# Kernel optimization log

Hardware: AMD Instinct MI355X
Metric: run time of the kernel (lower is better)

The kernel has to match this reference:

```python
import jax, jax.numpy as jnp
import numpy as np

EMB = 64      # per-head dim (emb_dim in source)
HEADS = 8
D = EMB * HEADS          # 512, model width
FF = 4 * EMB             # 256 (source uses ff_hidden_mult*emb_dim, not *D)
BS, NE = 32, 512
EPS = 1e-5


def _layernorm(x, g, b):
    mu = jnp.mean(x, axis=-1, keepdims=True)
    var = jnp.mean((x - mu) ** 2, axis=-1, keepdims=True)
    return (x - mu) * jax.lax.rsqrt(var + EPS) * g + b


def setup_inputs() -> dict:
    key = jax.random.key(0)
    ks = jax.random.split(key, 8)
    w = lambda k, shape: jax.random.normal(k, shape, jnp.float32) * 0.02
    return {
        "x": jax.random.normal(ks[0], (BS, NE, D), jnp.float32),
        "Wq": w(ks[1], (D, D)), "bq": jnp.zeros((D,), jnp.float32),
        "Wk": w(ks[2], (D, D)), "bk": jnp.zeros((D,), jnp.float32),
        "Wv": w(ks[3], (D, D)), "bv": jnp.zeros((D,), jnp.float32),
        "W1": w(ks[4], (D, FF)), "bf1": jnp.zeros((FF,), jnp.float32),
        "W2": w(ks[5], (FF, D)), "bf2": jnp.zeros((D,), jnp.float32),
        "g1": jnp.ones((D,), jnp.float32), "be1": jnp.zeros((D,), jnp.float32),
        "g2": jnp.ones((D,), jnp.float32), "be2": jnp.zeros((D,), jnp.float32),
    }


def reference(x, Wq, bq, Wk, bk, Wv, bv, W1, bf1, W2, bf2, g1, be1, g2, be2):
    bs, ne, _ = x.shape
    # --- SelfAttention.forward_i (manual multi-head attention) ---
    q = (x @ Wq + bq).reshape(bs, ne, HEADS, EMB)
    k = (x @ Wk + bk).reshape(bs, ne, HEADS, EMB)
    v = (x @ Wv + bv).reshape(bs, ne, HEADS, EMB)
    scores = jnp.einsum("bqhd,bkhd->bhqk", q, k) / jnp.sqrt(jnp.float32(EMB))
    att = jax.nn.softmax(scores, axis=-1)
    attended = jnp.einsum("bhqk,bkhd->bqhd", att, v).reshape(bs * ne, D)
    # --- TransformerBlock residual + LN + FF + LN ---
    xf = x.reshape(bs * ne, D)
    h = _layernorm(attended + xf, g1, be1)
    ff = jnp.maximum(h @ W1 + bf1, 0.0) @ W2 + bf2
    return _layernorm(ff + h, g2, be2)
```

## Files before the change

kernel.cpp:

```cpp
#include <hip/hip_runtime.h>

#define BS 32
#define NE 512
#define DMODEL 512
#define HEADS 8
#define EMB 64
#define FFH 256
#define MTOK (BS*NE)

typedef unsigned short u16;
typedef short v8s __attribute__((ext_vector_type(8)));
typedef float f32x4 __attribute__((ext_vector_type(4)));
typedef u16 u16x4 __attribute__((ext_vector_type(4)));

#define GLOAD16(G, L) \
  __builtin_amdgcn_global_load_lds((const __attribute__((address_space(1))) unsigned int*)(G), \
      (__attribute__((address_space(3))) unsigned int*)(L), 16, 0, 0)

static __device__ __forceinline__ unsigned cvt_pk_bf16(float lo, float hi) {
    unsigned r;
    asm("v_cvt_pk_bf16_f32 %0, %1, %2" : "=v"(r) : "v"(lo), "v"(hi));
    return r;
}

static __device__ __forceinline__ u16 f2bf_bits(float f) {
    unsigned u = __float_as_uint(f);
    u += 0x7fffu + ((u >> 16) & 1u);
    return (u16)(u >> 16);
}
static __device__ __forceinline__ float bflo(unsigned w) { return __uint_as_float(w << 16); }
static __device__ __forceinline__ float bfhi(unsigned w) { return __uint_as_float(w & 0xffff0000u); }

__global__ __launch_bounds__(256) void cvt_all_kernel(
    const float* __restrict__ x, u16* __restrict__ xb,
    const float* __restrict__ Wq, const float* __restrict__ Wk, const float* __restrict__ Wv,
    const float* __restrict__ W1, const float* __restrict__ W2,
    u16* __restrict__ WqkvT, u16* __restrict__ W1T, u16* __restrict__ W2T)
{
    const int id = blockIdx.x;
    const int tt = threadIdx.x;
    if (id < 8192) {
        int i = id*256 + tt;
        float4 v = ((const float4*)x)[i];
        u16x4 o = { f2bf_bits(v.x), f2bf_bits(v.y), f2bf_bits(v.z), f2bf_bits(v.w) };
        ((u16x4*)xb)[i] = o;
        return;
    }
    __shared__ float T[32][33];
    const int tid2 = id - 8192;
    const float* src; u16* dst; int ldsrc, lddst, sr, sc;
    if (tid2 < 768) {
        int w = tid2 >> 8, t = tid2 & 255;
        int tr = t >> 4, tc = t & 15;
        src = (w == 0) ? Wq : (w == 1) ? Wk : Wv;
        ldsrc = 512; sr = tr*32; sc = tc*32;
        dst = WqkvT + (size_t)(w*512 + sc)*512 + sr; lddst = 512;
    } else if (tid2 < 896) {
        int t = tid2 - 768;
        int tr = t >> 3, tc = t & 7;
        src = W1; ldsrc = 256; sr = tr*32; sc = tc*32;
        dst = W1T + (size_t)sc*512 + sr; lddst = 512;
    } else {
        int t = tid2 - 896;
        int tr = t >> 4, tc = t & 15;
        src = W2; ldsrc = 512; sr = tr*32; sc = tc*32;
        dst = W2T + (size_t)sc*256 + sr; lddst = 256;
    }
    {
        int r = tt >> 3, c4 = (tt & 7) << 2;
        float4 v = *(const float4*)(src + (size_t)(sr + r)*ldsrc + sc + c4);
        T[r][c4] = v.x; T[r][c4+1] = v.y; T[r][c4+2] = v.z; T[r][c4+3] = v.w;
    }
    __syncthreads();
    {
        int n = tt >> 3, k4 = (tt & 7) << 2;
        u16x4 o = { f2bf_bits(T[k4][n]), f2bf_bits(T[k4+1][n]),
                    f2bf_bits(T[k4+2][n]), f2bf_bits(T[k4+3][n]) };
        *(u16x4*)(dst + (size_t)n*lddst + k4) = o;
    }
}

__global__ __launch_bounds__(256, 2) void qkv_kernel(
    const u16* __restrict__ A, const u16* __restrict__ BT,
    const float* __restrict__ bsQ, const float* __restrict__ bsK, const float* __restrict__ bsV,
    u16* __restrict__ oQ, u16* __restrict__ oK, u16* __restrict__ oVT)
{
    __shared__ u16 Ab[2][128*64];
    __shared__ u16 Bb[2][128*64];
    const int tid = threadIdx.x;
    const int wave = tid >> 6, lane = tid & 63;
    const int lr = lane & 15, lg = lane >> 4, lr7 = lr & 7;
    const int id = blockIdx.x;
    const int rr = id & 7, qq = id >> 3;
    const int gk = qq / 12, colBlk = qq - gk*12;
    const int rowBlk = gk*8 + rr;
    const int aRow0 = rowBlk*128, bRow0 = colBlk*128;
    const int wlo = (wave >> 1)*64, wco = (wave & 1)*64;
    const int srow = tid >> 3, schunk = tid & 7;
    const int soff = ((schunk ^ (srow & 7)) << 3);
    const bool isV = (bRow0 >= 1024);

    auto stage = [&](int bsel, int k0) {
        #pragma unroll
        for (int i = 0; i < 4; ++i) {
            int row = i*32 + srow;
            GLOAD16(A  + (size_t)(aRow0 + row)*512 + k0 + soff, (char*)&Ab[bsel][0] + i*4096 + wave*1024);
            GLOAD16(BT + (size_t)(bRow0 + row)*512 + k0 + soff, (char*)&Bb[bsel][0] + i*4096 + wave*1024);
        }
    };

    stage(0, 0);

    f32x4 acc[4][4] = {};
    #pragma unroll
    for (int t = 0; t < 8; ++t) {
        const int cur = t & 1;
        asm volatile("s_waitcnt vmcnt(0)" ::: "memory");
        __builtin_amdgcn_s_barrier();
        if (t + 1 < 8) stage(cur ^ 1, (t + 1) * 64);
        #pragma unroll
        for (int kk = 0; kk < 2; ++kk) {
            v8s af[4], bf[4];
            #pragma unroll
            for (int i = 0; i < 4; ++i) {
                af[i] = *(const v8s*)((const char*)&Ab[cur][0] + (wlo + i*16 + lr)*128 + ((((kk<<2)|lg) ^ lr7) << 4));
                bf[i] = *(const v8s*)((const char*)&Bb[cur][0] + (wco + i*16 + lr)*128 + ((((kk<<2)|lg) ^ lr7) << 4));
            }
            if (isV) {
                #pragma unroll
                for (int i = 0; i < 4; ++i)
                    #pragma unroll
                    for (int j = 0; j < 4; ++j)
                        acc[i][j] = __builtin_amdgcn_mfma_f32_16x16x32_bf16(af[i], bf[j], acc[i][j], 0, 0, 0);
            } else {
                #pragma unroll
                for (int i = 0; i < 4; ++i)
                    #pragma unroll
                    for (int j = 0; j < 4; ++j)
                        acc[i][j] = __builtin_amdgcn_mfma_f32_16x16x32_bf16(bf[j], af[i], acc[i][j], 0, 0, 0);
            }
        }
    }

    if (isV) {
        #pragma unroll
        for (int j = 0; j < 4; ++j) {
            int col = (bRow0 & 511) + wco + j*16 + lr;
            float bv = bsV[col];
            int hh = col >> 6, d = col & 63;
            #pragma unroll
            for (int i = 0; i < 4; ++i) {
                int t0 = aRow0 + wlo + i*16 + lg*4;
                int bb = t0 >> 9, tr = t0 & 511;
                unsigned lo = cvt_pk_bf16(acc[i][j][0] + bv, acc[i][j][1] + bv);
                unsigned hi = cvt_pk_bf16(acc[i][j][2] + bv, acc[i][j][3] + bv);
                *(uint2*)(oVT + ((size_t)((bb*HEADS + hh)*EMB + d))*NE + tr) = make_uint2(lo, hi);
            }
        }
    } else {
        const int sel = (bRow0 >> 9) & 1;
        u16* dst = sel ? oK : oQ;
        const float* bias = sel ? bsK : bsQ;
        const int cb = bRow0 & 511;
        #pragma unroll
        for (int j = 0; j < 4; ++j) {
            int col0 = cb + wco + j*16 + lg*4;
            float4 b4 = *(const float4*)&bias[col0];
            #pragma unroll
            for (int i = 0; i < 4; ++i) {
                int row = aRow0 + wlo + i*16 + lr;
                float v0 = acc[i][j][0] + b4.x, v1 = acc[i][j][1] + b4.y;
                float v2 = acc[i][j][2] + b4.z, v3 = acc[i][j][3] + b4.w;
                if (sel == 0) {
                    const float SCL = 0.18033688011112042f;
                    v0 *= SCL; v1 *= SCL; v2 *= SCL; v3 *= SCL;
                }
                *(uint2*)(dst + (size_t)row*DMODEL + col0)
                    = make_uint2(cvt_pk_bf16(v0, v1), cvt_pk_bf16(v2, v3));
            }
        }
    }
}

__global__ __launch_bounds__(512, 2) void attn_kernel(
    const u16* __restrict__ Q, const u16* __restrict__ Kb,
    const u16* __restrict__ VT, u16* __restrict__ O)
{
    extern __shared__ char smem[];
    const int b = blockIdx.x >> 3, h = blockIdx.x & 7;
    const int tid = threadIdx.x, wave = tid >> 6, lane = tid & 63;
    const int lr = lane & 15, lg = lane >> 4, lr7 = lr & 7;

    const int srow = tid >> 3, schunk = tid & 7;
    const int soff = ((schunk ^ (srow & 7)) << 3);
    #pragma unroll
    for (int i = 0; i < 8; ++i)
        GLOAD16(Kb + (size_t)(b*NE + i*64 + srow)*DMODEL + h*EMB + soff,
                (char*)smem + i*8192 + wave*1024);
    #pragma unroll
    for (int i = 0; i < 8; ++i) {
        int row = i*8 + wave;
        GLOAD16(VT + (size_t)((b*HEADS + h)*EMB + row)*NE + lane*8,
                (char*)smem + 65536 + row*1040);
    }

    const int q0 = wave*64;
    v8s qa[4][2];
    #pragma unroll
    for (int ti = 0; ti < 4; ++ti) {
        const u16* qr = Q + (size_t)(b*NE + q0 + ti*16 + lr)*DMODEL + h*EMB;
        qa[ti][0] = *(const v8s*)(qr + lg*8);
        qa[ti][1] = *(const v8s*)(qr + 32 + lg*8);
    }
    __syncthreads();

    f32x4 o[4][4] = {};
    float ssum[4] = {0.f, 0.f, 0.f, 0.f};

    #pragma unroll 1
    for (int c = 0; c < 16; ++c) {
        const char* kr0 = (const char*)smem + ((2*c  )*16 + lr)*128;
        const char* kr1 = (const char*)smem + ((2*c+1)*16 + lr)*128;
        v8s kA0 = *(const v8s*)(kr0 + ((lg ^ lr7) << 4));
        v8s kA1 = *(const v8s*)(kr0 + (((4|lg) ^ lr7) << 4));
        v8s kB0 = *(const v8s*)(kr1 + ((lg ^ lr7) << 4));
        v8s kB1 = *(const v8s*)(kr1 + (((4|lg) ^ lr7) << 4));
        v8s vf[4];
        #pragma unroll
        for (int dt = 0; dt < 4; ++dt) {
            const char* vr = (const char*)smem + 65536 + (dt*16 + lr)*1040 + c*64 + lg*8;
            uint2 lo = *(const uint2*)(vr);
            uint2 hi = *(const uint2*)(vr + 32);
            uint4 u = make_uint4(lo.x, lo.y, hi.x, hi.y);
            vf[dt] = *(v8s*)&u;
        }
        #pragma unroll
        for (int ti = 0; ti < 4; ++ti) {
            __builtin_amdgcn_s_setprio(1);
            f32x4 s0 = {0.f,0.f,0.f,0.f}, s1 = {0.f,0.f,0.f,0.f};
            s0 = __builtin_amdgcn_mfma_f32_16x16x32_bf16(kA0, qa[ti][0], s0, 0, 0, 0);
            s0 = __builtin_amdgcn_mfma_f32_16x16x32_bf16(kA1, qa[ti][1], s0, 0, 0, 0);
            s1 = __builtin_amdgcn_mfma_f32_16x16x32_bf16(kB0, qa[ti][0], s1, 0, 0, 0);
            s1 = __builtin_amdgcn_mfma_f32_16x16x32_bf16(kB1, qa[ti][1], s1, 0, 0, 0);
            __builtin_amdgcn_s_setprio(0);
            float p0 = exp2f(s0[0]), p1 = exp2f(s0[1]), p2 = exp2f(s0[2]), p3 = exp2f(s0[3]);
            float r0 = exp2f(s1[0]), r1 = exp2f(s1[1]), r2 = exp2f(s1[2]), r3 = exp2f(s1[3]);
            ssum[ti] += ((p0 + p1) + (p2 + p3)) + ((r0 + r1) + (r2 + r3));
            unsigned a0 = cvt_pk_bf16(p0, p1), a1 = cvt_pk_bf16(p2, p3);
            unsigned b0 = cvt_pk_bf16(r0, r1), b1 = cvt_pk_bf16(r2, r3);
            uint4 pu = make_uint4(a0, a1, b0, b1);
            v8s pb = *(v8s*)&pu;
            __builtin_amdgcn_s_setprio(1);
            #pragma unroll
            for (int dt = 0; dt < 4; ++dt)
                o[ti][dt] = __builtin_amdgcn_mfma_f32_16x16x32_bf16(vf[dt], pb, o[ti][dt], 0, 0, 0);
            __builtin_amdgcn_s_setprio(0);
        }
    }

    __syncthreads();

    float rinv[4];
    #pragma unroll
    for (int ti = 0; ti < 4; ++ti) {
        float v = ssum[ti];
        v += __shfl_xor(v, 16);
        v += __shfl_xor(v, 32);
        rinv[ti] = 1.f / v;
    }

    char* ow = (char*)smem + wave*10240;
    #pragma unroll
    for (int ti = 0; ti < 4; ++ti) {
        #pragma unroll
        for (int dt = 0; dt < 4; ++dt) {
            unsigned d0 = cvt_pk_bf16(o[ti][dt][0]*rinv[ti], o[ti][dt][1]*rinv[ti]);
            unsigned d1 = cvt_pk_bf16(o[ti][dt][2]*rinv[ti], o[ti][dt][3]*rinv[ti]);
            *(uint2*)(ow + (ti*16 + lr)*160 + dt*32 + lg*8) = make_uint2(d0, d1);
        }
    }
    __asm__ volatile("s_waitcnt lgkmcnt(0)" ::: "memory");
    #pragma unroll
    for (int it = 0; it < 8; ++it) {
        int rr2 = it*8 + (lane >> 3);
        uint4 v = *(const uint4*)(ow + rr2*160 + (lane & 7)*16);
        *(uint4*)(O + (size_t)(b*NE + q0 + rr2)*DMODEL + h*EMB + (lane & 7)*8) = v;
    }
}

__global__ __launch_bounds__(512) void ffln_kernel(
    const u16* __restrict__ At, const u16* __restrict__ xb,
    const float* __restrict__ g1, const float* __restrict__ be1,
    const u16* __restrict__ W1T, const float* __restrict__ b1,
    const u16* __restrict__ W2T, const float* __restrict__ b2,
    const float* __restrict__ g2, const float* __restrict__ be2,
    float* __restrict__ out)
{
    extern __shared__ char smem[];
    char* H    = smem;
    char* F1   = smem + 65536;
    char* BSTa = smem + 98304;
    float* Ps = (float*)(smem + 131072);
    float* Pq = Ps + 128;

    const int tid = threadIdx.x, wave = tid >> 6, lane = tid & 63;
    const int lr = lane & 15, lg = lane >> 4, lr7 = lr & 7;
    const int r0 = blockIdx.x * 64;

    #pragma unroll
    for (int it = 0; it < 8; ++it) {
        int r = wave*8 + it;
        uint4 av = *(const uint4*)(At + (size_t)(r0 + r)*512 + lane*8);
        uint4 xv = *(const uint4*)(xb + (size_t)(r0 + r)*512 + lane*8);
        float v0 = bflo(av.x) + bflo(xv.x), v1 = bfhi(av.x) + bfhi(xv.x);
        float v2 = bflo(av.y) + bflo(xv.y), v3 = bfhi(av.y) + bfhi(xv.y);
        float v4 = bflo(av.z) + bflo(xv.z), v5 = bfhi(av.z) + bfhi(xv.z);
        float v6 = bflo(av.w) + bflo(xv.w), v7 = bfhi(av.w) + bfhi(xv.w);
        float s = ((v0+v1)+(v2+v3)) + ((v4+v5)+(v6+v7));
        float q = ((v0*v0+v1*v1)+(v2*v2+v3*v3)) + ((v4*v4+v5*v5)+(v6*v6+v7*v7));
        #pragma unroll
        for (int d = 1; d < 64; d <<= 1) { s += __shfl_xor(s, d); q += __shfl_xor(q, d); }
        float mu = s * (1.f/512.f);
        float rs = rsqrtf(q * (1.f/512.f) - mu*mu + 1e-5f);
        float4 gA = *(const float4*)(g1 + lane*8), gB = *(const float4*)(g1 + lane*8 + 4);
        float4 eA = *(const float4*)(be1 + lane*8), eB = *(const float4*)(be1 + lane*8 + 4);
        float h0 = (v0-mu)*rs*gA.x + eA.x, h1 = (v1-mu)*rs*gA.y + eA.y;
        float h2 = (v2-mu)*rs*gA.z + eA.z, h3 = (v3-mu)*rs*gA.w + eA.w;
        float h4 = (v4-mu)*rs*gB.x + eB.x, h5 = (v5-mu)*rs*gB.y + eB.y;
        float h6 = (v6-mu)*rs*gB.z + eB.z, h7 = (v7-mu)*rs*gB.w + eB.w;
        uint4 hw = make_uint4(cvt_pk_bf16(h0,h1), cvt_pk_bf16(h2,h3),
                              cvt_pk_bf16(h4,h5), cvt_pk_bf16(h6,h7));
        *(uint4*)(H + r*1024 + ((lane ^ (r & 7)) << 4)) = hw;
    }
    __syncthreads();

    const int wr = (wave & 3)*16, wcB = (wave >> 2)*128;

    auto stageW1 = [&](char* buf, int s8) {
        int k0 = s8*64;
        #pragma unroll
        for (int i = 0; i < 4; ++i) {
            int slot = i*512 + tid;
            int row = slot >> 3, ch = slot & 7;
            GLOAD16(W1T + (size_t)row*512 + k0 + ((ch ^ (row & 7)) << 3),
                    buf + i*8192 + wave*1024);
        }
    };
    stageW1(BSTa, 0);
    f32x4 acc1[8] = {};
    #pragma unroll
    for (int s8 = 0; s8 < 8; ++s8) {
        char* cur = (s8 & 1) ? F1 : BSTa;
        asm volatile("s_waitcnt vmcnt(0)" ::: "memory");
        __builtin_amdgcn_s_barrier();
        if (s8 + 1 < 8) stageW1((s8 & 1) ? BSTa : F1, s8 + 1);
        #pragma unroll
        for (int kk = 0; kk < 2; ++kk) {
            v8s af = *(const v8s*)(H + (wr + lr)*1024 + (((s8*8 + kk*4 + lg) ^ lr7) << 4));
            v8s bf[8];
            #pragma unroll
            for (int j = 0; j < 8; ++j)
                bf[j] = *(const v8s*)(cur + (wcB + j*16 + lr)*128 + ((((kk<<2)|lg) ^ lr7) << 4));
            #pragma unroll
            for (int j = 0; j < 8; ++j)
                acc1[j] = __builtin_amdgcn_mfma_f32_16x16x32_bf16(bf[j], af, acc1[j], 0, 0, 0);
        }
    }
    __syncthreads();

    {
        int row = wr + lr;
        #pragma unroll
        for (int j = 0; j < 8; ++j) {
            int col0 = wcB + j*16 + lg*4;
            float4 b4 = *(const float4*)(b1 + col0);
            float v0 = fmaxf(acc1[j][0] + b4.x, 0.f), v1 = fmaxf(acc1[j][1] + b4.y, 0.f);
            float v2 = fmaxf(acc1[j][2] + b4.z, 0.f), v3 = fmaxf(acc1[j][3] + b4.w, 0.f);
            *(uint2*)(F1 + row*512 + (((col0 >> 3) ^ (row & 7)) << 4) + (col0 & 7)*2)
                = make_uint2(cvt_pk_bf16(v0, v1), cvt_pk_bf16(v2, v3));
        }
    }

    const int row = wr + lr;
    uint2 hres[2][8];
    #pragma unroll
    for (int nh = 0; nh < 2; ++nh)
        #pragma unroll
        for (int j = 0; j < 8; ++j) {
            int col0 = nh*256 + wcB + j*16 + lg*4;
            hres[nh][j] = *(const uint2*)(H + row*1024 +
                            ((((col0 & 511) >> 3) ^ (row & 7)) << 4) + (col0 & 7)*2);
        }
    __syncthreads();

    auto stageW2 = [&](char* buf, int g) {
        int nh = g >> 2, k0 = (g & 3)*64;
        #pragma unroll
        for (int i = 0; i < 4; ++i) {
            int slot = i*512 + tid;
            int rw = slot >> 3, ch = slot & 7;
            GLOAD16(W2T + (size_t)(nh*256 + rw)*256 + k0 + ((ch ^ (rw & 7)) << 3),
                    buf + i*8192 + wave*1024);
        }
    };
    stageW2(H, 0);
    f32x4 acc2[2][8] = {};
    #pragma unroll
    for (int g = 0; g < 8; ++g) {
        char* cur = (g & 1) ? (H + 32768) : H;
        asm volatile("s_waitcnt vmcnt(0)" ::: "memory");
        __builtin_amdgcn_s_barrier();
        if (g + 1 < 8) stageW2((g & 1) ? H : (H + 32768), g + 1);
        const int nh = g >> 2, s4 = g & 3;
        #pragma unroll
        for (int kk = 0; kk < 2; ++kk) {
            v8s af = *(const v8s*)(F1 + (wr + lr)*512 + (((s4*8 + kk*4 + lg) ^ lr7) << 4));
            v8s bf[8];
            #pragma unroll
            for (int j = 0; j < 8; ++j)
                bf[j] = *(const v8s*)(cur + (wcB + j*16 + lr)*128 + ((((kk<<2)|lg) ^ lr7) << 4));
            #pragma unroll
            for (int j = 0; j < 8; ++j)
                acc2[nh][j] = __builtin_amdgcn_mfma_f32_16x16x32_bf16(bf[j], af, acc2[nh][j], 0, 0, 0);
        }
    }

    float s = 0.f, q = 0.f;
    #pragma unroll
    for (int nh = 0; nh < 2; ++nh) {
        #pragma unroll
        for (int j = 0; j < 8; ++j) {
            int col0 = nh*256 + wcB + j*16 + lg*4;
            float4 b4 = *(const float4*)(b2 + col0);
            uint2 hh = hres[nh][j];
            f32x4 a = acc2[nh][j];
            a[0] += b4.x + bflo(hh.x); a[1] += b4.y + bfhi(hh.x);
            a[2] += b4.z + bflo(hh.y); a[3] += b4.w + bfhi(hh.y);
            acc2[nh][j] = a;
            s += (a[0]+a[1]) + (a[2]+a[3]);
            q += (a[0]*a[0]+a[1]*a[1]) + (a[2]*a[2]+a[3]*a[3]);
        }
    }
    s += __shfl_xor(s, 16); s += __shfl_xor(s, 32);
    q += __shfl_xor(q, 16); q += __shfl_xor(q, 32);
    __syncthreads();
    if (lg == 0) { Ps[row*2 + (wave >> 2)] = s; Pq[row*2 + (wave >> 2)] = q; }
    __syncthreads();
    float st = Ps[row*2] + Ps[row*2 + 1];
    float qt = Pq[row*2] + Pq[row*2 + 1];
    float mu = st * (1.f/512.f);
    float rs = rsqrtf(qt * (1.f/512.f) - mu*mu + 1e-5f);

    #pragma unroll
    for (int nh = 0; nh < 2; ++nh) {
        #pragma unroll
        for (int j = 0; j < 8; ++j) {
            int col0 = nh*256 + wcB + j*16 + lg*4;
            float4 gg = *(const float4*)(g2 + col0);
            float4 ee = *(const float4*)(be2 + col0);
            f32x4 a = acc2[nh][j];
            float4 o;
            o.x = (a[0]-mu)*rs*gg.x + ee.x;
            o.y = (a[1]-mu)*rs*gg.y + ee.y;
            o.z = (a[2]-mu)*rs*gg.z + ee.z;
            o.w = (a[3]-mu)*rs*gg.w + ee.w;
            *(float4*)(out + (size_t)(r0 + row)*512 + col0) = o;
        }
    }
}


extern "C" void kernel_launch(void* const* d_in, const int* in_sizes, int n_in,
                              void* d_out, int out_size, void* d_ws, size_t ws_size,
                              hipStream_t stream)
{
    const float* x   = (const float*)d_in[0];
    const float* Wq  = (const float*)d_in[1];
    const float* bq  = (const float*)d_in[2];
    const float* Wk  = (const float*)d_in[3];
    const float* bk  = (const float*)d_in[4];
    const float* Wv  = (const float*)d_in[5];
    const float* bv  = (const float*)d_in[6];
    const float* W1  = (const float*)d_in[7];
    const float* bf1 = (const float*)d_in[8];
    const float* W2  = (const float*)d_in[9];
    const float* bf2 = (const float*)d_in[10];
    const float* g1  = (const float*)d_in[11];
    const float* be1 = (const float*)d_in[12];
    const float* g2  = (const float*)d_in[13];
    const float* be2 = (const float*)d_in[14];

    char* ws = (char*)d_ws;
    const size_t MB = 1ull << 20;
    const size_t KB = 1024;
    u16* xb    = (u16*)(ws + 0);
    u16* qb    = (u16*)(ws + 16*MB);
    u16* kb    = (u16*)(ws + 32*MB);
    u16* vT    = (u16*)(ws + 48*MB);
    u16* attnb = (u16*)(ws + 64*MB);
    u16* WqkvT = (u16*)(ws + 80*MB);
    u16* W1T   = (u16*)(ws + 80*MB + 1536*KB);
    u16* W2T   = (u16*)(ws + 80*MB + 1792*KB);
    (void)ws_size; (void)in_sizes; (void)n_in; (void)out_size;

    cvt_all_kernel<<<9216, 256, 0, stream>>>(x, xb, Wq, Wk, Wv, W1, W2, WqkvT, W1T, W2T);

    qkv_kernel<<<1536, 256, 0, stream>>>(xb, WqkvT, bq, bk, bv, qb, kb, vT);

    attn_kernel<<<256, 512, 132096, stream>>>(qb, kb, vT, attnb);

    ffln_kernel<<<256, 512, 132096, stream>>>(attnb, xb, g1, be1, W1T, bf1, W2T, bf2,
                                              g2, be2, (float*)d_out);
}
```

Measured before the change: 114.4 us.

## Fuse QKV projection into attention kernel using MFMA-fragment-packed inputs

Removes the separate QKV GEMM kernel and computes each head's Q, K and V projections inside the attention block. Q, K and V now go straight to LDS instead of round-tripping through global memory. To feed MFMA directly from global memory without LDS staging, x and Wqkv are repacked in the conversion kernel into a 16-row by 8-element fragment layout. Each block recomputes projections from global x with register double buffering. The trade-off is lower occupancy (launch bounds no longer request 2 blocks per CU), extra conversion writes, and global-load latency exposed inside the GEMM passes.

```diff
diff --git a/kernel.cpp b/kernel.cpp
--- a/kernel.cpp
+++ b/kernel.cpp
@@ -32,10 +32,10 @@
 static __device__ __forceinline__ float bfhi(unsigned w) { return __uint_as_float(w & 0xffff0000u); }
 
 __global__ __launch_bounds__(256) void cvt_all_kernel(
-    const float* __restrict__ x, u16* __restrict__ xb,
+    const float* __restrict__ x, u16* __restrict__ xb, u16* __restrict__ xp,
     const float* __restrict__ Wq, const float* __restrict__ Wk, const float* __restrict__ Wv,
     const float* __restrict__ W1, const float* __restrict__ W2,
-    u16* __restrict__ WqkvT, u16* __restrict__ W1T, u16* __restrict__ W2T)
+    u16* __restrict__ Wp, u16* __restrict__ W1T, u16* __restrict__ W2T)
 {
     const int id = blockIdx.x;
     const int tt = threadIdx.x;
@@ -44,24 +44,29 @@
         float4 v = ((const float4*)x)[i];
         u16x4 o = { f2bf_bits(v.x), f2bf_bits(v.y), f2bf_bits(v.z), f2bf_bits(v.w) };
         ((u16x4*)xb)[i] = o;
+        int e = i * 4;
+        int row = e >> 9, k = e & 511;
+        *(u16x4*)(xp + ((size_t)(row >> 4)*64 + (k >> 3))*128 + (row & 15)*8 + (k & 7)) = o;
         return;
     }
+    if (id < 11264) {
+        int widx = (id - 8192)*256 + tt;
+        int w = widx >> 18, rem = widx & 262143;
+        int k = rem >> 9, n = rem & 511;
+        const float* src = (w == 0) ? Wq : (w == 1) ? Wk : Wv;
+        int np = w*512 + n;
+        Wp[((size_t)(np >> 4)*64 + (k >> 3))*128 + (np & 15)*8 + (k & 7)] = f2bf_bits(src[rem]);
+        return;
+    }
     __shared__ float T[32][33];
-    const int tid2 = id - 8192;
+    const int t2 = id - 11264;
     const float* src; u16* dst; int ldsrc, lddst, sr, sc;
-    if (tid2 < 768) {
-        int w = tid2 >> 8, t = tid2 & 255;
-        int tr = t >> 4, tc = t & 15;
-        src = (w == 0) ? Wq : (w == 1) ? Wk : Wv;
-        ldsrc = 512; sr = tr*32; sc = tc*32;
-        dst = WqkvT + (size_t)(w*512 + sc)*512 + sr; lddst = 512;
-    } else if (tid2 < 896) {
-        int t = tid2 - 768;
-        int tr = t >> 3, tc = t & 7;
+    if (t2 < 128) {
+        int tr = t2 >> 3, tc = t2 & 7;
         src = W1; ldsrc = 256; sr = tr*32; sc = tc*32;
         dst = W1T + (size_t)sc*512 + sr; lddst = 512;
     } else {
-        int t = tid2 - 896;
+        int t = t2 - 128;
         int tr = t >> 4, tc = t & 15;
         src = W2; ldsrc = 512; sr = tr*32; sc = tc*32;
         dst = W2T + (size_t)sc*256 + sr; lddst = 256;
@@ -80,140 +85,118 @@
     }
 }
 
-__global__ __launch_bounds__(256, 2) void qkv_kernel(
-    const u16* __restrict__ A, const u16* __restrict__ BT,
+__global__ __launch_bounds__(512) void fused_attn_kernel(
+    const u16* __restrict__ xp, const u16* __restrict__ Wp,
     const float* __restrict__ bsQ, const float* __restrict__ bsK, const float* __restrict__ bsV,
-    u16* __restrict__ oQ, u16* __restrict__ oK, u16* __restrict__ oVT)
-{
-    __shared__ u16 Ab[2][128*64];
-    __shared__ u16 Bb[2][128*64];
-    const int tid = threadIdx.x;
-    const int wave = tid >> 6, lane = tid & 63;
-    const int lr = lane & 15, lg = lane >> 4, lr7 = lr & 7;
-    const int id = blockIdx.x;
-    const int rr = id & 7, qq = id >> 3;
-    const int gk = qq / 12, colBlk = qq - gk*12;
-    const int rowBlk = gk*8 + rr;
-    const int aRow0 = rowBlk*128, bRow0 = colBlk*128;
-    const int wlo = (wave >> 1)*64, wco = (wave & 1)*64;
-    const int srow = tid >> 3, schunk = tid & 7;
-    const int soff = ((schunk ^ (srow & 7)) << 3);
-    const bool isV = (bRow0 >= 1024);
-
-    auto stage = [&](int bsel, int k0) {
-        #pragma unroll
-        for (int i = 0; i < 4; ++i) {
-            int row = i*32 + srow;
-            GLOAD16(A  + (size_t)(aRow0 + row)*512 + k0 + soff, (char*)&Ab[bsel][0] + i*4096 + wave*1024);
-            GLOAD16(BT + (size_t)(bRow0 + row)*512 + k0 + soff, (char*)&Bb[bsel][0] + i*4096 + wave*1024);
-        }
-    };
-
-    stage(0, 0);
-
-    f32x4 acc[4][4] = {};
-    #pragma unroll
-    for (int t = 0; t < 8; ++t) {
-        const int cur = t & 1;
-        asm volatile("s_waitcnt vmcnt(0)" ::: "memory");
-        __builtin_amdgcn_s_barrier();
-        if (t + 1 < 8) stage(cur ^ 1, (t + 1) * 64);
-        #pragma unroll
-        for (int kk = 0; kk < 2; ++kk) {
-            v8s af[4], bf[4];
-            #pragma unroll
-            for (int i = 0; i < 4; ++i) {
-                af[i] = *(const v8s*)((const char*)&Ab[cur][0] + (wlo + i*16 + lr)*128 + ((((kk<<2)|lg) ^ lr7) << 4));
-                bf[i] = *(const v8s*)((const char*)&Bb[cur][0] + (wco + i*16 + lr)*128 + ((((kk<<2)|lg) ^ lr7) << 4));
-            }
-            if (isV) {
-                #pragma unroll
-                for (int i = 0; i < 4; ++i)
-                    #pragma unroll
-                    for (int j = 0; j < 4; ++j)
-                        acc[i][j] = __builtin_amdgcn_mfma_f32_16x16x32_bf16(af[i], bf[j], acc[i][j], 0, 0, 0);
-            } else {
-                #pragma unroll
-                for (int i = 0; i < 4; ++i)
-                    #pragma unroll
-                    for (int j = 0; j < 4; ++j)
-                        acc[i][j] = __builtin_amdgcn_mfma_f32_16x16x32_bf16(bf[j], af[i], acc[i][j], 0, 0, 0);
-            }
-        }
-    }
-
-    if (isV) {
-        #pragma unroll
-        for (int j = 0; j < 4; ++j) {
-            int col = (bRow0 & 511) + wco + j*16 + lr;
-            float bv = bsV[col];
-            int hh = col >> 6, d = col & 63;
-            #pragma unroll
-            for (int i = 0; i < 4; ++i) {
-                int t0 = aRow0 + wlo + i*16 + lg*4;
-                int bb = t0 >> 9, tr = t0 & 511;
-                unsigned lo = cvt_pk_bf16(acc[i][j][0] + bv, acc[i][j][1] + bv);
-                unsigned hi = cvt_pk_bf16(acc[i][j][2] + bv, acc[i][j][3] + bv);
-                *(uint2*)(oVT + ((size_t)((bb*HEADS + hh)*EMB + d))*NE + tr) = make_uint2(lo, hi);
-            }
-        }
-    } else {
-        const int sel = (bRow0 >> 9) & 1;
-        u16* dst = sel ? oK : oQ;
-        const float* bias = sel ? bsK : bsQ;
-        const int cb = bRow0 & 511;
-        #pragma unroll
-        for (int j = 0; j < 4; ++j) {
-            int col0 = cb + wco + j*16 + lg*4;
-            float4 b4 = *(const float4*)&bias[col0];
-            #pragma unroll
-            for (int i = 0; i < 4; ++i) {
-                int row = aRow0 + wlo + i*16 + lr;
-                float v0 = acc[i][j][0] + b4.x, v1 = acc[i][j][1] + b4.y;
-                float v2 = acc[i][j][2] + b4.z, v3 = acc[i][j][3] + b4.w;
-                if (sel == 0) {
-                    const float SCL = 0.18033688011112042f;
-                    v0 *= SCL; v1 *= SCL; v2 *= SCL; v3 *= SCL;
-                }
-                *(uint2*)(dst + (size_t)row*DMODEL + col0)
-                    = make_uint2(cvt_pk_bf16(v0, v1), cvt_pk_bf16(v2, v3));
-            }
-        }
-    }
-}
-
-__global__ __launch_bounds__(512, 2) void attn_kernel(
-    const u16* __restrict__ Q, const u16* __restrict__ Kb,
-    const u16* __restrict__ VT, u16* __restrict__ O)
+    u16* __restrict__ O)
 {
     extern __shared__ char smem[];
     const int b = blockIdx.x >> 3, h = blockIdx.x & 7;
     const int tid = threadIdx.x, wave = tid >> 6, lane = tid & 63;
     const int lr = lane & 15, lg = lane >> 4, lr7 = lr & 7;
-
-    const int srow = tid >> 3, schunk = tid & 7;
-    const int soff = ((schunk ^ (srow & 7)) << 3);
-    #pragma unroll
-    for (int i = 0; i < 8; ++i)
-        GLOAD16(Kb + (size_t)(b*NE + i*64 + srow)*DMODEL + h*EMB + soff,
-                (char*)smem + i*8192 + wave*1024);
-    #pragma unroll
-    for (int i = 0; i < 8; ++i) {
-        int row = i*8 + wave;
-        GLOAD16(VT + (size_t)((b*HEADS + h)*EMB + row)*NE + lane*8,
-                (char*)smem + 65536 + row*1040);
-    }
+    char* Bnc = smem + 65536;
+    const float SCL = 0.18033688011112042f;
+
+    const u16* a0  = xp + ((size_t)(b*32 + wave*4)*64 + lg)*128 + lr*8;
+    const u16* bq0 = Wp + ((size_t)(h*4      )*64 + lg)*128 + lr*8;
+    const u16* bk0 = Wp + ((size_t)(32 + h*4 )*64 + lg)*128 + lr*8;
+    const u16* bv0 = Wp + ((size_t)(64 + h*4 )*64 + lg)*128 + lr*8;
+
+    f32x4 acc[4][4];
+
+    auto run_pass = [&](const u16* bb, bool swap) {
+        #pragma unroll
+        for (int i = 0; i < 4; ++i)
+            #pragma unroll
+            for (int j = 0; j < 4; ++j) acc[i][j] = f32x4{0.f,0.f,0.f,0.f};
+        v8s afA[4], bfA[4], afB[4], bfB[4];
+        #pragma unroll
+        for (int i = 0; i < 4; ++i) { afA[i] = *(const v8s*)(a0 + i*8192); bfA[i] = *(const v8s*)(bb + i*8192); }
+        #pragma unroll
+        for (int tp = 0; tp < 8; ++tp) {
+            #pragma unroll
+            for (int i = 0; i < 4; ++i) {
+                afB[i] = *(const v8s*)(a0 + (2*tp + 1)*512 + i*8192);
+                bfB[i] = *(const v8s*)(bb + (2*tp + 1)*512 + i*8192);
+            }
+            #pragma unroll
+            for (int i = 0; i < 4; ++i)
+                #pragma unroll
+                for (int j = 0; j < 4; ++j)
+                    acc[i][j] = swap
+                        ? __builtin_amdgcn_mfma_f32_16x16x32_bf16(bfA[j], afA[i], acc[i][j], 0, 0, 0)
+                        : __builtin_amdgcn_mfma_f32_16x16x32_bf16(afA[i], bfA[j], acc[i][j], 0, 0, 0);
+            if (tp < 7) {
+                #pragma unroll
+                for (int i = 0; i < 4; ++i) {
+                    afA[i] = *(const v8s*)(a0 + (2*tp + 2)*512 + i*8192);
+                    bfA[i] = *(const v8s*)(bb + (2*tp + 2)*512 + i*8192);
+                }
+            }
+            #pragma unroll
+            for (int i = 0; i < 4; ++i)
+                #pragma unroll
+                for (int j = 0; j < 4; ++j)
+                    acc[i][j] = swap
+                        ? __builtin_amdgcn_mfma_f32_16x16x32_bf16(bfB[j], afB[i], acc[i][j], 0, 0, 0)
+                        : __builtin_amdgcn_mfma_f32_16x16x32_bf16(afB[i], bfB[j], acc[i][j], 0, 0, 0);
+        }
+    };
+
+    run_pass(bq0, true);
+    #pragma unroll
+    for (int j = 0; j < 4; ++j) {
+        float4 b4 = *(const float4*)(bsQ + h*64 + j*16 + lg*4);
+        #pragma unroll
+        for (int i = 0; i < 4; ++i) {
+            int tok = wave*64 + i*16 + lr;
+            float v0 = (acc[i][j][0] + b4.x)*SCL, v1 = (acc[i][j][1] + b4.y)*SCL;
+            float v2 = (acc[i][j][2] + b4.z)*SCL, v3 = (acc[i][j][3] + b4.w)*SCL;
+            int chunk = 2*j + (lg >> 1);
+            *(uint2*)(Bnc + tok*128 + ((chunk ^ lr7) << 4) + (lg & 1)*8)
+                = make_uint2(cvt_pk_bf16(v0, v1), cvt_pk_bf16(v2, v3));
+        }
+    }
+    v8s qa[4][2];
+    #pragma unroll
+    for (int ti = 0; ti < 4; ++ti) {
+        const char* qr = Bnc + (wave*64 + ti*16 + lr)*128;
+        qa[ti][0] = *(const v8s*)(qr + ((lg ^ lr7) << 4));
+        qa[ti][1] = *(const v8s*)(qr + (((4 | lg) ^ lr7) << 4));
+    }
+
+    run_pass(bk0, true);
+    #pragma unroll
+    for (int j = 0; j < 4; ++j) {
+        float4 b4 = *(const float4*)(bsK + h*64 + j*16 + lg*4);
+        #pragma unroll
+        for (int i = 0; i < 4; ++i) {
+            int tok = wave*64 + i*16 + lr;
+            float v0 = acc[i][j][0] + b4.x, v1 = acc[i][j][1] + b4.y;
+            float v2 = acc[i][j][2] + b4.z, v3 = acc[i][j][3] + b4.w;
+            int chunk = 2*j + (lg >> 1);
+            *(uint2*)(smem + tok*128 + ((chunk ^ lr7) << 4) + (lg & 1)*8)
+                = make_uint2(cvt_pk_bf16(v0, v1), cvt_pk_bf16(v2, v3));
+        }
+    }
+    __syncthreads();
+
+    run_pass(bv0, false);
+    #pragma unroll
+    for (int j = 0; j < 4; ++j) {
+        #pragma unroll
+        for (int i = 0; i < 4; ++i) {
+            int d = j*16 + lr;
+            float bv = bsV[h*64 + d];
+            int chunk = wave*8 + 2*i + (lg >> 1);
+            *(uint2*)(Bnc + d*1024 + ((chunk ^ lr7) << 4) + (lg & 1)*8)
+                = make_uint2(cvt_pk_bf16(acc[i][j][0] + bv, acc[i][j][1] + bv),
+                             cvt_pk_bf16(acc[i][j][2] + bv, acc[i][j][3] + bv));
+        }
+    }
+    __syncthreads();
 
     const int q0 = wave*64;
-    v8s qa[4][2];
-    #pragma unroll
-    for (int ti = 0; ti < 4; ++ti) {
-        const u16* qr = Q + (size_t)(b*NE + q0 + ti*16 + lr)*DMODEL + h*EMB;
-        qa[ti][0] = *(const v8s*)(qr + lg*8);
-        qa[ti][1] = *(const v8s*)(qr + 32 + lg*8);
-    }
-    __syncthreads();
-
     f32x4 o[4][4] = {};
     float ssum[4] = {0.f, 0.f, 0.f, 0.f};
 
@@ -228,9 +211,10 @@
         v8s vf[4];
         #pragma unroll
         for (int dt = 0; dt < 4; ++dt) {
-            const char* vr = (const char*)smem + 65536 + (dt*16 + lr)*1040 + c*64 + lg*8;
-            uint2 lo = *(const uint2*)(vr);
-            uint2 hi = *(const uint2*)(vr + 32);
+            const char* vr = Bnc + (dt*16 + lr)*1024;
+            int c0 = c*4 + (lg >> 1), rem = (lg & 1)*8;
+            uint2 lo = *(const uint2*)(vr + (((c0    ) ^ lr7) << 4) + rem);
+            uint2 hi = *(const uint2*)(vr + (((c0 + 2) ^ lr7) << 4) + rem);
             uint4 u = make_uint4(lo.x, lo.y, hi.x, hi.y);
             vf[dt] = *(v8s*)&u;
         }
@@ -246,9 +230,9 @@
             float p0 = exp2f(s0[0]), p1 = exp2f(s0[1]), p2 = exp2f(s0[2]), p3 = exp2f(s0[3]);
             float r0 = exp2f(s1[0]), r1 = exp2f(s1[1]), r2 = exp2f(s1[2]), r3 = exp2f(s1[3]);
             ssum[ti] += ((p0 + p1) + (p2 + p3)) + ((r0 + r1) + (r2 + r3));
-            unsigned a0 = cvt_pk_bf16(p0, p1), a1 = cvt_pk_bf16(p2, p3);
-            unsigned b0 = cvt_pk_bf16(r0, r1), b1 = cvt_pk_bf16(r2, r3);
-            uint4 pu = make_uint4(a0, a1, b0, b1);
+            unsigned a0w = cvt_pk_bf16(p0, p1), a1w = cvt_pk_bf16(p2, p3);
+            unsigned b0w = cvt_pk_bf16(r0, r1), b1w = cvt_pk_bf16(r2, r3);
+            uint4 pu = make_uint4(a0w, a1w, b0w, b1w);
             v8s pb = *(v8s*)&pu;
             __builtin_amdgcn_s_setprio(1);
             #pragma unroll
@@ -494,20 +478,16 @@
     const size_t MB = 1ull << 20;
     const size_t KB = 1024;
     u16* xb    = (u16*)(ws + 0);
-    u16* qb    = (u16*)(ws + 16*MB);
-    u16* kb    = (u16*)(ws + 32*MB);
-    u16* vT    = (u16*)(ws + 48*MB);
-    u16* attnb = (u16*)(ws + 64*MB);
-    u16* WqkvT = (u16*)(ws + 80*MB);
-    u16* W1T   = (u16*)(ws + 80*MB + 1536*KB);
-    u16* W2T   = (u16*)(ws + 80*MB + 1792*KB);
+    u16* xp    = (u16*)(ws + 16*MB);
+    u16* attnb = (u16*)(ws + 32*MB);
+    u16* Wp    = (u16*)(ws + 48*MB);
+    u16* W1T   = (u16*)(ws + 48*MB + 1536*KB);
+    u16* W2T   = (u16*)(ws + 48*MB + 1792*KB);
     (void)ws_size; (void)in_sizes; (void)n_in; (void)out_size;
 
-    cvt_all_kernel<<<9216, 256, 0, stream>>>(x, xb, Wq, Wk, Wv, W1, W2, WqkvT, W1T, W2T);
-
-    qkv_kernel<<<1536, 256, 0, stream>>>(xb, WqkvT, bq, bk, bv, qb, kb, vT);
-
-    attn_kernel<<<256, 512, 132096, stream>>>(qb, kb, vT, attnb);
+    cvt_all_kernel<<<11520, 256, 0, stream>>>(x, xb, xp, Wq, Wk, Wv, W1, W2, Wp, W1T, W2T);
+
+    fused_attn_kernel<<<256, 512, 131072, stream>>>(xp, Wp, bq, bk, bv, attnb);
 
     ffln_kernel<<<256, 512, 132096, stream>>>(attnb, xb, g1, be1, W1T, bf1, W2T, bf2,
                                               g2, be2, (float*)d_out);
```

New measurement: 137.4 us. 20.1% more time.
